# Kernel tuning notes

Hardware: AMD Instinct MI355X
Metric: run time of the kernel (lower is better)

## Reference

```python
import jax, jax.numpy as jnp
import numpy as np

N_NODES = 40000

def setup_inputs() -> dict:
    key = jax.random.key(0)
    k1, k2, k3, k4 = jax.random.split(key, 4)
    x = jax.random.normal(k1, (N_NODES, 256), dtype=jnp.float32)
    edge_index = jax.random.randint(k2, (2, 640000), 0, N_NODES, dtype=jnp.int64)
    W = jax.random.normal(k3, (256, 128), dtype=jnp.float32) * (1.0 / np.sqrt(256))
    b = jax.random.normal(k4, (128,), dtype=jnp.float32) * 0.01
    return {"x": x, "edge_index": edge_index, "W": W, "b": b}

def reference(x, edge_index, W, b):
    N = x.shape[0]
    # GCNConv: add self-loops, symmetric degree normalization, linear, aggregate, bias
    loops = jnp.arange(N, dtype=edge_index.dtype)
    src = jnp.concatenate([edge_index[0], loops])  # message sources j
    dst = jnp.concatenate([edge_index[1], loops])  # targets i
    ones = jnp.ones_like(dst, dtype=x.dtype)
    deg = jax.ops.segment_sum(ones, dst, num_segments=N)  # in-degree incl. self-loop
    dinv = jnp.where(deg > 0, jax.lax.rsqrt(deg), 0.0)
    norm = dinv[src] * dinv[dst]  # [E+N]
    xw = x @ W  # transform first (in_dim -> out_dim), as in PyG GCNConv
    msgs = norm[:, None] * xw[src]  # [E+N, out_dim]
    agg = jax.ops.segment_sum(msgs, dst, num_segments=N) + b
    return jax.nn.relu(agg)  # dropout_value == 0 -> no dropout
```

## Files before the change

### kernel.cpp

```cpp
#include <hip/hip_runtime.h>

#define N_NODES 40000
#define IN_DIM 256
#define OUT_DIM 128
#define CAP 64
#define GEMM_BLOCKS 625
#define FILL_BLOCKS 625

typedef __bf16 bf16x8 __attribute__((ext_vector_type(8)));
typedef float floatx4 __attribute__((ext_vector_type(4)));

__device__ __forceinline__ int clamp_idx(int v) {
    unsigned u = (unsigned)v;
    return (u < (unsigned)N_NODES) ? v : 0;
}

__device__ __forceinline__ int ld_edge(const int* e32, long long idx, int is64) {
    return is64 ? e32[2 * idx] : e32[idx];
}

__device__ __forceinline__ float bflo(unsigned u) {
    union { unsigned i; float f; } c; c.i = u << 16; return c.f;
}
__device__ __forceinline__ float bfhi(unsigned u) {
    union { unsigned i; float f; } c; c.i = u & 0xFFFF0000u; return c.f;
}

__global__ void prep_r16(const int* __restrict__ edge32, int* __restrict__ flag,
                         int* __restrict__ cnt, const float* __restrict__ W,
                         __bf16* __restrict__ wswz) {
    int i = blockIdx.x * 256 + threadIdx.x;
    if (i < N_NODES) cnt[i] = 0;
    if (i < IN_DIM * OUT_DIM) {
        int j    = i & 7;
        int lane = (i >> 3) & 63;
        int tile = i >> 9;
        int ct = tile & 7, kc = tile >> 3;
        int k = kc * 32 + (lane >> 4) * 8 + j;
        int n = ct * 16 + (lane & 15);
        wswz[i] = (__bf16)W[k * OUT_DIM + n];
    }
    if (blockIdx.x == 0) {
        __shared__ int sh[256];
        int t = threadIdx.x;
        int nz = 0;
        for (int k = t; k < 1000; k += 256) nz |= (edge32[2 * k + 1] != 0);
        sh[t] = nz;
        __syncthreads();
        for (int off = 128; off > 0; off >>= 1) {
            if (t < off) sh[t] |= sh[t + off];
            __syncthreads();
        }
        if (t == 0) *flag = sh[0] ? 0 : 1;
    }
}

__global__ __launch_bounds__(256) void gemm_r16(
    const float* __restrict__ x, const __bf16* __restrict__ wswz,
    __bf16* __restrict__ xwb) {
    int t = threadIdx.x;
    int wave = t >> 6, lane = t & 63;
    int quad = lane >> 4, m16 = lane & 15;
    int m = blockIdx.x * 64 + wave * 16 + m16;
    const float* xrow = x + (long long)m * IN_DIM;
    const bf16x8* wp = (const bf16x8*)wswz;

    floatx4 acc[8];
#pragma unroll
    for (int ct = 0; ct < 8; ++ct) acc[ct] = (floatx4){0.f, 0.f, 0.f, 0.f};

#pragma unroll
    for (int kc = 0; kc < 8; ++kc) {
        int k0 = kc * 32 + quad * 8;
        float4 xa = *(const float4*)(xrow + k0);
        float4 xb = *(const float4*)(xrow + k0 + 4);
        bf16x8 af;
        af[0] = (__bf16)xa.x; af[1] = (__bf16)xa.y;
        af[2] = (__bf16)xa.z; af[3] = (__bf16)xa.w;
        af[4] = (__bf16)xb.x; af[5] = (__bf16)xb.y;
        af[6] = (__bf16)xb.z; af[7] = (__bf16)xb.w;
#pragma unroll
        for (int ct = 0; ct < 8; ++ct) {
            bf16x8 bf = wp[(kc * 8 + ct) * 64 + lane];
            acc[ct] = __builtin_amdgcn_mfma_f32_16x16x32_bf16(af, bf, acc[ct], 0, 0, 0);
        }
    }

    unsigned* xwu = (unsigned*)xwb;
    int rbase = blockIdx.x * 64 + wave * 16 + quad * 4;
#pragma unroll
    for (int p = 0; p < 4; ++p) {
#pragma unroll
        for (int r = 0; r < 4; ++r) {
            __bf16 lo = (__bf16)acc[2 * p][r];
            __bf16 hi = (__bf16)acc[2 * p + 1][r];
            unsigned u = ((unsigned)__builtin_bit_cast(unsigned short, hi) << 16)
                       | (unsigned)__builtin_bit_cast(unsigned short, lo);
            xwu[(long long)(rbase + r) * 64 + p * 16 + m16] = u;
        }
    }
}

__global__ __launch_bounds__(256) void fill_r16(
    const void* __restrict__ edge, int E, const int* __restrict__ flag,
    int* __restrict__ cnt, unsigned short* __restrict__ bucket) {
    int is64 = *flag;
    const int* e32 = (const int*)edge;
    long long base = (long long)blockIdx.x * 1024 + threadIdx.x * 4;
    int s0 = clamp_idx(ld_edge(e32, base + 0, is64));
    int s1 = clamp_idx(ld_edge(e32, base + 1, is64));
    int s2 = clamp_idx(ld_edge(e32, base + 2, is64));
    int s3 = clamp_idx(ld_edge(e32, base + 3, is64));
    int d0 = clamp_idx(ld_edge(e32, E + base + 0, is64));
    int d1 = clamp_idx(ld_edge(e32, E + base + 1, is64));
    int d2 = clamp_idx(ld_edge(e32, E + base + 2, is64));
    int d3 = clamp_idx(ld_edge(e32, E + base + 3, is64));
    int p0 = atomicAdd(&cnt[d0], 1);
    int p1 = atomicAdd(&cnt[d1], 1);
    int p2 = atomicAdd(&cnt[d2], 1);
    int p3 = atomicAdd(&cnt[d3], 1);
    if (p0 < CAP) bucket[d0 * CAP + p0] = (unsigned short)s0;
    if (p1 < CAP) bucket[d1 * CAP + p1] = (unsigned short)s1;
    if (p2 < CAP) bucket[d2 * CAP + p2] = (unsigned short)s2;
    if (p3 < CAP) bucket[d3 * CAP + p3] = (unsigned short)s3;
}

__global__ void gather_r16(const unsigned short* __restrict__ bucket,
                           const int* __restrict__ cnt,
                           const unsigned* __restrict__ xwd, const float* __restrict__ b,
                           float* __restrict__ out) {
    int node = blockIdx.x * 4 + (threadIdx.x >> 6);
    int lane = threadIdx.x & 63;
    if (node >= N_NODES) return;
    int cc = (lane >> 4) * 32 + (lane & 15);
    float b0 = b[cc], b1 = b[cc + 16];
    int cn_true = cnt[node];
    int take = cn_true < CAP ? cn_true : CAP;
    float dd = rsqrtf((float)(cn_true + 1));
    unsigned us = xwd[node * 64 + lane];
    float a0 = dd * dd * bflo(us);
    float a1 = dd * dd * bfhi(us);

    int s_l = 0; float nrm_l = 0.0f;
    if (lane < take) {
        s_l = (int)bucket[node * CAP + lane];
        nrm_l = dd * rsqrtf((float)(cnt[s_l] + 1));
    }
    int j = 0;
    for (; j + 8 <= take; j += 8) {
        int   s0 = __shfl(s_l, j),     s1 = __shfl(s_l, j + 1);
        int   s2 = __shfl(s_l, j + 2), s3 = __shfl(s_l, j + 3);
        int   s4 = __shfl(s_l, j + 4), s5 = __shfl(s_l, j + 5);
        int   s6 = __shfl(s_l, j + 6), s7 = __shfl(s_l, j + 7);
        float n0 = __shfl(nrm_l, j),     n1 = __shfl(nrm_l, j + 1);
        float n2 = __shfl(nrm_l, j + 2), n3 = __shfl(nrm_l, j + 3);
        float n4 = __shfl(nrm_l, j + 4), n5 = __shfl(nrm_l, j + 5);
        float n6 = __shfl(nrm_l, j + 6), n7 = __shfl(nrm_l, j + 7);
        unsigned u0 = xwd[s0 * 64 + lane], u1 = xwd[s1 * 64 + lane];
        unsigned u2 = xwd[s2 * 64 + lane], u3 = xwd[s3 * 64 + lane];
        unsigned u4 = xwd[s4 * 64 + lane], u5 = xwd[s5 * 64 + lane];
        unsigned u6 = xwd[s6 * 64 + lane], u7 = xwd[s7 * 64 + lane];
        a0 += n0 * bflo(u0); a1 += n0 * bfhi(u0);
        a0 += n1 * bflo(u1); a1 += n1 * bfhi(u1);
        a0 += n2 * bflo(u2); a1 += n2 * bfhi(u2);
        a0 += n3 * bflo(u3); a1 += n3 * bfhi(u3);
        a0 += n4 * bflo(u4); a1 += n4 * bfhi(u4);
        a0 += n5 * bflo(u5); a1 += n5 * bfhi(u5);
        a0 += n6 * bflo(u6); a1 += n6 * bfhi(u6);
        a0 += n7 * bflo(u7); a1 += n7 * bfhi(u7);
    }
    for (; j < take; ++j) {
        int   s = __shfl(s_l, j);
        float n = __shfl(nrm_l, j);
        unsigned u = xwd[s * 64 + lane];
        a0 += n * bflo(u); a1 += n * bfhi(u);
    }
    out[(long long)node * OUT_DIM + cc]      = fmaxf(a0 + b0, 0.0f);
    out[(long long)node * OUT_DIM + cc + 16] = fmaxf(a1 + b1, 0.0f);
}

extern "C" void kernel_launch(void* const* d_in, const int* in_sizes, int n_in,
                              void* d_out, int out_size, void* d_ws, size_t ws_size,
                              hipStream_t stream) {
    const float* x   = (const float*)d_in[0];
    const void* edge = d_in[1];
    const float* W   = (const float*)d_in[2];
    const float* b   = (const float*)d_in[3];
    float* out       = (float*)d_out;

    int E = in_sizes[1] / 2;

    char* ws = (char*)d_ws;
    int*            cnt    = (int*)(ws);
    int*            flag   = (int*)(ws + 160000);
    __bf16*         wswz   = (__bf16*)(ws + 160256);
    unsigned short* bucket = (unsigned short*)(ws + 225792);
    __bf16*         xwb    = (__bf16*)(ws + 5345792);

    prep_r16<<<160, 256, 0, stream>>>((const int*)edge, flag, cnt, W, wswz);
    fill_r16<<<FILL_BLOCKS, 256, 0, stream>>>(edge, E, flag, cnt, bucket);
    gemm_r16<<<GEMM_BLOCKS, 256, 0, stream>>>(x, wswz, xwb);
    gather_r16<<<N_NODES / 4, 256, 0, stream>>>(bucket, cnt, (const unsigned*)xwb, b, out);
}
```

Baseline: 160.3 us.

## Fuse GEMM and edge bucketing into one launch and pad degree counters

The separate GEMM and edge-fill kernels become one launch whose block index picks the role, so the compute-bound MFMA work and the atomic-bound bucketing can run at the same time on the GPU. The per-node degree counters are spread out to one per 128 bytes to cut atomic contention on shared cache lines. A new small compaction kernel copies the padded counters into a dense degree array for the gather. This adds a 5 MB padded counter buffer, more zeroing traffic, and an extra launch.

```diff
diff --git a/kernel.cpp b/kernel.cpp
--- a/kernel.cpp
+++ b/kernel.cpp
@@ -26,11 +26,11 @@
     union { unsigned i; float f; } c; c.i = u & 0xFFFF0000u; return c.f;
 }
 
-__global__ void prep_r16(const int* __restrict__ edge32, int* __restrict__ flag,
-                         int* __restrict__ cnt, const float* __restrict__ W,
+__global__ void prep_r18(const int* __restrict__ edge32, int* __restrict__ flag,
+                         int* __restrict__ cnt_pad, const float* __restrict__ W,
                          __bf16* __restrict__ wswz) {
     int i = blockIdx.x * 256 + threadIdx.x;
-    if (i < N_NODES) cnt[i] = 0;
+    if (i < N_NODES) cnt_pad[i << 5] = 0;
     if (i < IN_DIM * OUT_DIM) {
         int j    = i & 7;
         int lane = (i >> 3) & 63;
@@ -55,78 +55,83 @@
     }
 }
 
-__global__ __launch_bounds__(256) void gemm_r16(
+__global__ __launch_bounds__(256) void main_r18(
     const float* __restrict__ x, const __bf16* __restrict__ wswz,
-    __bf16* __restrict__ xwb) {
+    __bf16* __restrict__ xwb,
+    const void* __restrict__ edge, int E, const int* __restrict__ flag,
+    int* __restrict__ cnt_pad, unsigned short* __restrict__ bucket) {
     int t = threadIdx.x;
-    int wave = t >> 6, lane = t & 63;
-    int quad = lane >> 4, m16 = lane & 15;
-    int m = blockIdx.x * 64 + wave * 16 + m16;
-    const float* xrow = x + (long long)m * IN_DIM;
-    const bf16x8* wp = (const bf16x8*)wswz;
-
-    floatx4 acc[8];
-#pragma unroll
-    for (int ct = 0; ct < 8; ++ct) acc[ct] = (floatx4){0.f, 0.f, 0.f, 0.f};
-
-#pragma unroll
-    for (int kc = 0; kc < 8; ++kc) {
-        int k0 = kc * 32 + quad * 8;
-        float4 xa = *(const float4*)(xrow + k0);
-        float4 xb = *(const float4*)(xrow + k0 + 4);
-        bf16x8 af;
-        af[0] = (__bf16)xa.x; af[1] = (__bf16)xa.y;
-        af[2] = (__bf16)xa.z; af[3] = (__bf16)xa.w;
-        af[4] = (__bf16)xb.x; af[5] = (__bf16)xb.y;
-        af[6] = (__bf16)xb.z; af[7] = (__bf16)xb.w;
-#pragma unroll
-        for (int ct = 0; ct < 8; ++ct) {
-            bf16x8 bf = wp[(kc * 8 + ct) * 64 + lane];
-            acc[ct] = __builtin_amdgcn_mfma_f32_16x16x32_bf16(af, bf, acc[ct], 0, 0, 0);
+    if (blockIdx.x < GEMM_BLOCKS) {
+        int wave = t >> 6, lane = t & 63;
+        int quad = lane >> 4, m16 = lane & 15;
+        int m = blockIdx.x * 64 + wave * 16 + m16;
+        const float* xrow = x + (long long)m * IN_DIM;
+        const bf16x8* wp = (const bf16x8*)wswz;
+
+        floatx4 acc[8];
+#pragma unroll
+        for (int ct = 0; ct < 8; ++ct) acc[ct] = (floatx4){0.f, 0.f, 0.f, 0.f};
+
+#pragma unroll
+        for (int kc = 0; kc < 8; ++kc) {
+            int k0 = kc * 32 + quad * 8;
+            float4 xa = *(const float4*)(xrow + k0);
+            float4 xb = *(const float4*)(xrow + k0 + 4);
+            bf16x8 af;
+            af[0] = (__bf16)xa.x; af[1] = (__bf16)xa.y;
+            af[2] = (__bf16)xa.z; af[3] = (__bf16)xa.w;
+            af[4] = (__bf16)xb.x; af[5] = (__bf16)xb.y;
+            af[6] = (__bf16)xb.z; af[7] = (__bf16)xb.w;
+#pragma unroll
+            for (int ct = 0; ct < 8; ++ct) {
+                bf16x8 bf = wp[(kc * 8 + ct) * 64 + lane];
+                acc[ct] = __builtin_amdgcn_mfma_f32_16x16x32_bf16(af, bf, acc[ct], 0, 0, 0);
+            }
         }
-    }
-
-    unsigned* xwu = (unsigned*)xwb;
-    int rbase = blockIdx.x * 64 + wave * 16 + quad * 4;
-#pragma unroll
-    for (int p = 0; p < 4; ++p) {
-#pragma unroll
-        for (int r = 0; r < 4; ++r) {
-            __bf16 lo = (__bf16)acc[2 * p][r];
-            __bf16 hi = (__bf16)acc[2 * p + 1][r];
-            unsigned u = ((unsigned)__builtin_bit_cast(unsigned short, hi) << 16)
-                       | (unsigned)__builtin_bit_cast(unsigned short, lo);
-            xwu[(long long)(rbase + r) * 64 + p * 16 + m16] = u;
+
+        unsigned* xwu = (unsigned*)xwb;
+        int rbase = blockIdx.x * 64 + wave * 16 + quad * 4;
+#pragma unroll
+        for (int p = 0; p < 4; ++p) {
+#pragma unroll
+            for (int r = 0; r < 4; ++r) {
+                __bf16 lo = (__bf16)acc[2 * p][r];
+                __bf16 hi = (__bf16)acc[2 * p + 1][r];
+                unsigned u = ((unsigned)__builtin_bit_cast(unsigned short, hi) << 16)
+                           | (unsigned)__builtin_bit_cast(unsigned short, lo);
+                xwu[(long long)(rbase + r) * 64 + p * 16 + m16] = u;
+            }
         }
-    }
-}
-
-__global__ __launch_bounds__(256) void fill_r16(
-    const void* __restrict__ edge, int E, const int* __restrict__ flag,
-    int* __restrict__ cnt, unsigned short* __restrict__ bucket) {
-    int is64 = *flag;
-    const int* e32 = (const int*)edge;
-    long long base = (long long)blockIdx.x * 1024 + threadIdx.x * 4;
-    int s0 = clamp_idx(ld_edge(e32, base + 0, is64));
-    int s1 = clamp_idx(ld_edge(e32, base + 1, is64));
-    int s2 = clamp_idx(ld_edge(e32, base + 2, is64));
-    int s3 = clamp_idx(ld_edge(e32, base + 3, is64));
-    int d0 = clamp_idx(ld_edge(e32, E + base + 0, is64));
-    int d1 = clamp_idx(ld_edge(e32, E + base + 1, is64));
-    int d2 = clamp_idx(ld_edge(e32, E + base + 2, is64));
-    int d3 = clamp_idx(ld_edge(e32, E + base + 3, is64));
-    int p0 = atomicAdd(&cnt[d0], 1);
-    int p1 = atomicAdd(&cnt[d1], 1);
-    int p2 = atomicAdd(&cnt[d2], 1);
-    int p3 = atomicAdd(&cnt[d3], 1);
-    if (p0 < CAP) bucket[d0 * CAP + p0] = (unsigned short)s0;
-    if (p1 < CAP) bucket[d1 * CAP + p1] = (unsigned short)s1;
-    if (p2 < CAP) bucket[d2 * CAP + p2] = (unsigned short)s2;
-    if (p3 < CAP) bucket[d3 * CAP + p3] = (unsigned short)s3;
-}
-
-__global__ void gather_r16(const unsigned short* __restrict__ bucket,
-                           const int* __restrict__ cnt,
+    } else {
+        int is64 = *flag;
+        const int* e32 = (const int*)edge;
+        long long base = (long long)(blockIdx.x - GEMM_BLOCKS) * 1024 + t * 4;
+        int s0 = clamp_idx(ld_edge(e32, base + 0, is64));
+        int s1 = clamp_idx(ld_edge(e32, base + 1, is64));
+        int s2 = clamp_idx(ld_edge(e32, base + 2, is64));
+        int s3 = clamp_idx(ld_edge(e32, base + 3, is64));
+        int d0 = clamp_idx(ld_edge(e32, E + base + 0, is64));
+        int d1 = clamp_idx(ld_edge(e32, E + base + 1, is64));
+        int d2 = clamp_idx(ld_edge(e32, E + base + 2, is64));
+        int d3 = clamp_idx(ld_edge(e32, E + base + 3, is64));
+        int p0 = atomicAdd(&cnt_pad[d0 << 5], 1);
+        int p1 = atomicAdd(&cnt_pad[d1 << 5], 1);
+        int p2 = atomicAdd(&cnt_pad[d2 << 5], 1);
+        int p3 = atomicAdd(&cnt_pad[d3 << 5], 1);
+        if (p0 < CAP) bucket[d0 * CAP + p0] = (unsigned short)s0;
+        if (p1 < CAP) bucket[d1 * CAP + p1] = (unsigned short)s1;
+        if (p2 < CAP) bucket[d2 * CAP + p2] = (unsigned short)s2;
+        if (p3 < CAP) bucket[d3 * CAP + p3] = (unsigned short)s3;
+    }
+}
+
+__global__ void compact_r18(const int* __restrict__ cnt_pad, int* __restrict__ deg) {
+    int i = blockIdx.x * 256 + threadIdx.x;
+    if (i < N_NODES) deg[i] = cnt_pad[i << 5];
+}
+
+__global__ void gather_r18(const unsigned short* __restrict__ bucket,
+                           const int* __restrict__ deg,
                            const unsigned* __restrict__ xwd, const float* __restrict__ b,
                            float* __restrict__ out) {
     int node = blockIdx.x * 4 + (threadIdx.x >> 6);
@@ -134,7 +139,7 @@
     if (node >= N_NODES) return;
     int cc = (lane >> 4) * 32 + (lane & 15);
     float b0 = b[cc], b1 = b[cc + 16];
-    int cn_true = cnt[node];
+    int cn_true = deg[node];
     int take = cn_true < CAP ? cn_true : CAP;
     float dd = rsqrtf((float)(cn_true + 1));
     unsigned us = xwd[node * 64 + lane];
@@ -144,7 +149,7 @@
     int s_l = 0; float nrm_l = 0.0f;
     if (lane < take) {
         s_l = (int)bucket[node * CAP + lane];
-        nrm_l = dd * rsqrtf((float)(cnt[s_l] + 1));
+        nrm_l = dd * rsqrtf((float)(deg[s_l] + 1));
     }
     int j = 0;
     for (; j + 8 <= take; j += 8) {
@@ -191,14 +196,16 @@
     int E = in_sizes[1] / 2;
 
     char* ws = (char*)d_ws;
-    int*            cnt    = (int*)(ws);
-    int*            flag   = (int*)(ws + 160000);
-    __bf16*         wswz   = (__bf16*)(ws + 160256);
-    unsigned short* bucket = (unsigned short*)(ws + 225792);
-    __bf16*         xwb    = (__bf16*)(ws + 5345792);
-
-    prep_r16<<<160, 256, 0, stream>>>((const int*)edge, flag, cnt, W, wswz);
-    fill_r16<<<FILL_BLOCKS, 256, 0, stream>>>(edge, E, flag, cnt, bucket);
-    gemm_r16<<<GEMM_BLOCKS, 256, 0, stream>>>(x, wswz, xwb);
-    gather_r16<<<N_NODES / 4, 256, 0, stream>>>(bucket, cnt, (const unsigned*)xwb, b, out);
-}
+    int*            cnt_pad = (int*)(ws);
+    int*            flag    = (int*)(ws + 5120000);
+    int*            deg     = (int*)(ws + 5120256);
+    __bf16*         wswz    = (__bf16*)(ws + 5280256);
+    unsigned short* bucket  = (unsigned short*)(ws + 5345792);
+    __bf16*         xwb     = (__bf16*)(ws + 10465792);
+
+    prep_r18<<<160, 256, 0, stream>>>((const int*)edge, flag, cnt_pad, W, wswz);
+    main_r18<<<GEMM_BLOCKS + FILL_BLOCKS, 256, 0, stream>>>(
+        x, wswz, xwb, edge, E, flag, cnt_pad, bucket);
+    compact_r18<<<157, 256, 0, stream>>>(cnt_pad, deg);
+    gather_r18<<<N_NODES / 4, 256, 0, stream>>>(bucket, deg, (const unsigned*)xwb, b, out);
+}
```

Measured after the change: 154.4 us. 1.04x faster.
